# Kernel tuning notes

Hardware: AMD Instinct MI355X
Metric: run time of the kernel (lower is better)

The kernel has to match this reference:

```python
import jax, jax.numpy as jnp
import numpy as np

N = 50000        # nodes
E = 800000       # edges (avg degree 16)
C_IN = 128
H = 256          # hidden_channels
C_OUT = 128
DEPTH = 4
K = 2            # k_hops -> K+1 = 3 TAGConv weight matrices
L = DEPTH - 1    # residual layers after layer-0 conv
EPS = 1e-5
SLOPE = 0.01     # LeakyReLU default negative slope


def setup_inputs() -> dict:
    key = jax.random.key(0)
    ks = iter(jax.random.split(key, 24))
    s = 0.02
    x = jax.random.normal(next(ks), (N, C_IN), dtype=jnp.float32)
    edge_index = jax.random.randint(next(ks), (2, E), 0, N, dtype=jnp.int64)
    edge_weight = jax.random.uniform(next(ks), (E,), dtype=jnp.float32)
    return {
        'x': x,
        'edge_index': edge_index,
        'edge_weight': edge_weight,
        'W_emb': jax.random.normal(next(ks), (C_IN, H)) * s,
        'b_emb': jnp.zeros((H,), jnp.float32),
        'conv0_W': jax.random.normal(next(ks), (K + 1, H, H)) * s,
        'conv0_b': jnp.zeros((H,), jnp.float32),
        'norm_g': jnp.ones((L, H), jnp.float32),
        'norm_b': jnp.zeros((L, H), jnp.float32),
        'conv_W': jax.random.normal(next(ks), (L, K + 1, H, H)) * s,
        'conv_b': jnp.zeros((L, H), jnp.float32),
        'mlp_W1': jax.random.normal(next(ks), (L, H, 4 * H)) * s,
        'mlp_b1': jnp.zeros((L, 4 * H), jnp.float32),
        'mlp_g': jnp.ones((L, 4 * H), jnp.float32),
        'mlp_bb': jnp.zeros((L, 4 * H), jnp.float32),
        'mlp_W2': jax.random.normal(next(ks), (L, 4 * H, H)) * s,
        'mlp_b2': jnp.zeros((L, H), jnp.float32),
        'W_out': jax.random.normal(next(ks), (H, C_OUT)) * s,
        'b_out': jnp.zeros((C_OUT,), jnp.float32),
    }


def _bn(h, g, b):
    # BatchNorm1d over node dim (training-mode batch statistics)
    m = h.mean(axis=0)
    v = h.var(axis=0)
    return g * (h - m) * jax.lax.rsqrt(v + EPS) + b


def _tagconv(h, src, dst, ew, Ws, b):
    # TAGConv (normalize=False, no self loops): sum_k (A^k h) W_k + b
    out = h @ Ws[0]
    p = h
    for k in range(1, Ws.shape[0]):
        msg = p[src] * ew[:, None]                      # [E, H] gather
        p = jax.ops.segment_sum(msg, dst, num_segments=h.shape[0])
        out = out + p @ Ws[k]
    return out + b


def reference(x, edge_index, edge_weight, W_emb, b_emb, conv0_W, conv0_b,
              norm_g, norm_b, conv_W, conv_b, mlp_W1, mlp_b1, mlp_g, mlp_bb,
              mlp_W2, mlp_b2, W_out, b_out):
    src, dst = edge_index[0], edge_index[1]
    h = x @ W_emb + b_emb                               # x_embed (t=None)
    h = _tagconv(h, src, dst, edge_weight, conv0_W, conv0_b)  # layer-0 conv only
    for l in range(norm_g.shape[0]):                    # res+ blocks
        z = jax.nn.leaky_relu(_bn(h, norm_g[l], norm_b[l]), SLOPE)
        z = _tagconv(z, src, dst, edge_weight, conv_W[l], conv_b[l])
        # pyg MLP [H, 4H, H]: Linear -> BN -> act -> Linear (plain last)
        z = jax.nn.leaky_relu(_bn(z @ mlp_W1[l] + mlp_b1[l], mlp_g[l], mlp_bb[l]), SLOPE)
        z = z @ mlp_W2[l] + mlp_b2[l]
        h = h + z                                       # residual (res=Identity)
    return h @ W_out + b_out
```

## Files before the change

kernel.cpp:

```cpp
#include <hip/hip_runtime.h>

#define HDIM 256
#define EPSV 1e-5f
#define SLOPEV 0.01f

typedef __bf16 bf16;
typedef bf16  bf16x8 __attribute__((ext_vector_type(8)));
typedef bf16  bf16x4 __attribute__((ext_vector_type(4)));
typedef float f32x4  __attribute__((ext_vector_type(4)));

#define GLD16(g, l) __builtin_amdgcn_global_load_lds( \
    (const __attribute__((address_space(1))) void*)(g), \
    (__attribute__((address_space(3))) void*)(l), 16, 0, 0)

template<bool STORE_BF16, bool STATS, bool FUSE_BN>
__global__ __launch_bounds__(256, 5)
void gemm_bt_k(const bf16* A0, const bf16* A1, const bf16* A2, const bf16* A3,
               int nseg, int segK,
               const bf16* __restrict__ Wt,
               const float* __restrict__ bias, const bf16* __restrict__ addb,
               void* out0, void* out1, void* out2, void* out3, int ldo,
               int n_store, float* part, int n_stats,
               const float* __restrict__ fcoef)
{
    __shared__ char smem[24576];

    const int tid = threadIdx.x;
    const int wave = tid >> 6, lane = tid & 63;
    const int quad = lane >> 4, l16 = lane & 15;
    const int waveM = (wave >> 1) * 32, waveN = (wave & 1) * 64;

    int bid = blockIdx.y * gridDim.x + blockIdx.x;
    const int nwg = gridDim.x * gridDim.y;
    if ((nwg & 7) == 0) {
        const int cpx = nwg >> 3;
        bid = (bid & 7) * cpx + (bid >> 3);
    }
    const int bx = bid % gridDim.x, by = bid / gridDim.x;
    const int bm = by * 64, bn = bx * 128;
    const int K = nseg * segK;

    const bf16* segs[4] = {A0, A1, A2, A3};
    const int srow = tid >> 2;
    const int skof = (tid & 3) * 8;

    f32x4 acc[2][4] = {};

    const int T = K >> 5;

    bf16x8 aReg;
    float4 ca0, ca1, cd0, cd1;

    auto loadA = [&](int s, int kt) {
        const bf16* gA = segs[s] + (size_t)(bm + srow) * segK + kt + skof;
        aReg = *(const bf16x8*)gA;
        int g = s * segK + kt + skof;
        ca0 = *(const float4*)(fcoef + g);
        ca1 = *(const float4*)(fcoef + g + 4);
        cd0 = *(const float4*)(fcoef + K + g);
        cd1 = *(const float4*)(fcoef + K + g + 4);
    };
    auto applyA = [&](int b) {
        float av[8] = {ca0.x, ca0.y, ca0.z, ca0.w, ca1.x, ca1.y, ca1.z, ca1.w};
        float dv[8] = {cd0.x, cd0.y, cd0.z, cd0.w, cd1.x, cd1.y, cd1.z, cd1.w};
        bf16x8 z;
#pragma unroll
        for (int u = 0; u < 8; ++u) {
            float f = fmaf((float)aReg[u], av[u], dv[u]);
            f = f > 0.f ? f : SLOPEV * f;
            z[u] = (bf16)f;
        }
        *(bf16x8*)(smem + b * 4096 + tid * 16) = z;
    };
    auto stageA_lds = [&](int s, int kt, int b) {
        const bf16* gA = segs[s] + (size_t)(bm + srow) * segK + kt + skof;
        GLD16(gA, smem + b * 4096 + wave * 1024);
    };
    auto stageB = [&](int s, int kt, int b) {
        const bf16* gB = Wt + (size_t)(bn + srow) * K + s * segK + kt + skof;
        char* lB = smem + 8192 + b * 8192 + wave * 1024;
        GLD16(gB,                  lB);
        GLD16(gB + (size_t)64 * K, lB + 4096);
    };

    if (FUSE_BN) loadA(0, 0); else stageA_lds(0, 0, 0);
    stageB(0, 0, 0);
    if (FUSE_BN) applyA(0);
    __syncthreads();

    int s = 0, kt = 0;
    for (int t = 0; t < T; ++t) {
        int s2 = s, kt2 = kt + 32;
        if (kt2 == segK) { s2++; kt2 = 0; }
        if (t + 1 < T) {
            if (FUSE_BN) loadA(s2, kt2); else stageA_lds(s2, kt2, (t + 1) & 1);
            stageB(s2, kt2, (t + 1) & 1);
        }

        const bf16* pa = (const bf16*)(smem + (t & 1) * 4096)
                         + (waveM + l16) * 32 + quad * 8;
        const bf16* pb = (const bf16*)(smem + 8192 + (t & 1) * 8192)
                         + (waveN + l16) * 32 + quad * 8;
        bf16x8 a0 = *(const bf16x8*)(pa);
        bf16x8 a1 = *(const bf16x8*)(pa + 16 * 32);
        bf16x8 b0 = *(const bf16x8*)(pb);
        bf16x8 b1 = *(const bf16x8*)(pb + 16 * 32);
        bf16x8 b2 = *(const bf16x8*)(pb + 32 * 32);
        bf16x8 b3 = *(const bf16x8*)(pb + 48 * 32);

        acc[0][0] = __builtin_amdgcn_mfma_f32_16x16x32_bf16(a0, b0, acc[0][0], 0, 0, 0);
        acc[0][1] = __builtin_amdgcn_mfma_f32_16x16x32_bf16(a0, b1, acc[0][1], 0, 0, 0);
        acc[0][2] = __builtin_amdgcn_mfma_f32_16x16x32_bf16(a0, b2, acc[0][2], 0, 0, 0);
        acc[0][3] = __builtin_amdgcn_mfma_f32_16x16x32_bf16(a0, b3, acc[0][3], 0, 0, 0);
        acc[1][0] = __builtin_amdgcn_mfma_f32_16x16x32_bf16(a1, b0, acc[1][0], 0, 0, 0);
        acc[1][1] = __builtin_amdgcn_mfma_f32_16x16x32_bf16(a1, b1, acc[1][1], 0, 0, 0);
        acc[1][2] = __builtin_amdgcn_mfma_f32_16x16x32_bf16(a1, b2, acc[1][2], 0, 0, 0);
        acc[1][3] = __builtin_amdgcn_mfma_f32_16x16x32_bf16(a1, b3, acc[1][3], 0, 0, 0);

        if (FUSE_BN && t + 1 < T) applyA((t + 1) & 1);
        __syncthreads();
        s = s2; kt = kt2;
    }

    float bv[4];
#pragma unroll
    for (int j = 0; j < 4; ++j)
        bv[j] = bias ? bias[bn + waveN + j * 16 + l16] : 0.f;
#pragma unroll
    for (int i = 0; i < 2; ++i)
#pragma unroll
        for (int j = 0; j < 4; ++j)
#pragma unroll
            for (int r = 0; r < 4; ++r)
                acc[i][j][r] += bv[j];

    void* outs[4] = {out0, out1, out2, out3};

    if (STORE_BF16) {
        char* stg = smem + wave * 4608;
        float s8[8] = {}, q8[8] = {};
        const int rsel = lane >> 3, csel = lane & 7;
#pragma unroll
        for (int i = 0; i < 2; ++i)
#pragma unroll
            for (int j = 0; j < 4; ++j)
#pragma unroll
                for (int r = 0; r < 4; ++r)
                    *(bf16*)(stg + ((i * 16 + quad * 4 + r) * 72 + j * 16 + l16) * 2)
                        = (bf16)acc[i][j][r];
#pragma unroll
        for (int rr = 0; rr < 4; ++rr) {
            int rl = rsel + rr * 8;
            bf16x8 v = *(const bf16x8*)(stg + (rl * 72 + csel * 8) * 2);
            int rowg = bm + waveM + rl;
            int colg = bn + waveN + csel * 8;
            int cseg = colg >> 8, cloc = colg & 255;
            size_t idx = (size_t)rowg * ldo + cloc;
            float f[8];
#pragma unroll
            for (int u = 0; u < 8; ++u) f[u] = (float)v[u];
            if (addb) {
                bf16x8 o = *(const bf16x8*)(addb + idx);
#pragma unroll
                for (int u = 0; u < 8; ++u) f[u] += (float)o[u];
            }
            bf16x8 w;
#pragma unroll
            for (int u = 0; u < 8; ++u) w[u] = (bf16)f[u];
            if (rowg < n_store) *(bf16x8*)((bf16*)outs[cseg] + idx) = w;
            if (STATS && rowg < n_stats) {
#pragma unroll
                for (int u = 0; u < 8; ++u) { s8[u] += f[u]; q8[u] += f[u] * f[u]; }
            }
        }
        if (STATS) {
#pragma unroll
            for (int m = 8; m <= 32; m <<= 1)
#pragma unroll
                for (int u = 0; u < 8; ++u) {
                    s8[u] += __shfl_xor(s8[u], m, 64);
                    q8[u] += __shfl_xor(q8[u], m, 64);
                }
            float* Ls = (float*)(smem + 18432);
            float* Lq = Ls + 256;
            if (rsel == 0) {
#pragma unroll
                for (int u = 0; u < 8; ++u) {
                    Ls[wave * 64 + csel * 8 + u] = s8[u];
                    Lq[wave * 64 + csel * 8 + u] = q8[u];
                }
            }
            __syncthreads();
            if (tid < 128) {
                int hi = tid >> 6, c6 = tid & 63;
                float sv = Ls[hi * 64 + c6] + Ls[(hi + 2) * 64 + c6];
                float qv = Lq[hi * 64 + c6] + Lq[(hi + 2) * 64 + c6];
                int Mtot = gridDim.x * 128;
                int colg = bn + tid;
                part[(size_t)by * Mtot + colg] = sv;
                part[(size_t)(gridDim.y + by) * Mtot + colg] = qv;
            }
        }
    } else {
#pragma unroll
        for (int i = 0; i < 2; ++i)
#pragma unroll
            for (int j = 0; j < 4; ++j) {
                int colg = bn + waveN + j * 16 + l16;
                int cseg = colg >> 8, cloc = colg & 255;
#pragma unroll
                for (int r = 0; r < 4; ++r) {
                    int rowg = bm + waveM + i * 16 + quad * 4 + r;
                    if (rowg < n_store)
                        ((float*)outs[cseg])[(size_t)rowg * ldo + cloc] = acc[i][j][r];
                }
            }
    }
}

__global__ __launch_bounds__(256)
void finalize_k(const float* __restrict__ part, int GY, int M,
                const float* __restrict__ g, const float* __restrict__ bb,
                float* __restrict__ coef, float invn)
{
    const int c = blockIdx.x;
    const int t = threadIdx.x;
    float s = 0.f, q = 0.f;
    const float* ps = part + c;
    const float* pq = part + (size_t)GY * M + c;
    for (int i = t; i < GY; i += 256) {
        s += ps[(size_t)i * M];
        q += pq[(size_t)i * M];
    }
#pragma unroll
    for (int m = 1; m <= 32; m <<= 1) {
        s += __shfl_xor(s, m, 64);
        q += __shfl_xor(q, m, 64);
    }
    __shared__ float Ls[4], Lq[4];
    const int w = t >> 6, l = t & 63;
    if (l == 0) { Ls[w] = s; Lq[w] = q; }
    __syncthreads();
    if (t == 0) {
        s = Ls[0] + Ls[1] + Ls[2] + Ls[3];
        q = Lq[0] + Lq[1] + Lq[2] + Lq[3];
        float mean = s * invn;
        float var  = q * invn - mean * mean;
        float a = g[c] * rsqrtf(var + EPSV);
        coef[c]     = a;
        coef[M + c] = bb[c] - mean * a;
    }
}

__global__ __launch_bounds__(256)
void transpose_cvt_k(const float* __restrict__ src, bf16* __restrict__ dst,
                     int Kseg, int M, int G)
{
    __shared__ float t[32][33];
    const int z = blockIdx.z;
    src += (size_t)z * Kseg * M;
    const int ldd = G * Kseg;
    dst += (size_t)(z / G) * M * ldd + (size_t)(z % G) * Kseg;
    const int tM = blockIdx.x * 32, tK = blockIdx.y * 32;
    const int tx = threadIdx.x & 31, ty = threadIdx.x >> 5;
#pragma unroll
    for (int r = 0; r < 4; ++r)
        t[ty + r * 8][tx] = src[(size_t)(tK + ty + r * 8) * M + tM + tx];
    __syncthreads();
#pragma unroll
    for (int r = 0; r < 4; ++r)
        dst[(size_t)(tM + ty + r * 8) * ldd + tK + tx] = (bf16)t[tx][ty + r * 8];
}

__global__ __launch_bounds__(256)
void cvt_bf_k(const float* __restrict__ src, bf16* __restrict__ dst, long n4)
{
    long i = (long)blockIdx.x * blockDim.x + threadIdx.x;
    if (i >= n4) return;
    float4 v = ((const float4*)src)[i];
    bf16x4 o; o[0] = (bf16)v.x; o[1] = (bf16)v.y; o[2] = (bf16)v.z; o[3] = (bf16)v.w;
    ((bf16x4*)dst)[i] = o;
}

__global__ __launch_bounds__(256)
void deg_k(const int* __restrict__ dst, int* __restrict__ deg, int E)
{
    int e = blockIdx.x * blockDim.x + threadIdx.x;
    if (e < E) atomicAdd(&deg[dst[e]], 1);
}

__global__ __launch_bounds__(256)
void blocksum_k(const int* __restrict__ deg, int* __restrict__ bsum, int N)
{
    int i = blockIdx.x * 256 + threadIdx.x;
    int v = (i < N) ? deg[i] : 0;
#pragma unroll
    for (int m = 1; m <= 32; m <<= 1) v += __shfl_xor(v, m, 64);
    __shared__ int Ls[4];
    if ((threadIdx.x & 63) == 0) Ls[threadIdx.x >> 6] = v;
    __syncthreads();
    if (threadIdx.x == 0) bsum[blockIdx.x] = Ls[0] + Ls[1] + Ls[2] + Ls[3];
}

__global__ __launch_bounds__(256)
void topscan_k(const int* __restrict__ bsum, int* __restrict__ boff, int nb)
{
    __shared__ int s[256];
    int t = threadIdx.x;
    int v = (t < nb) ? bsum[t] : 0;
    s[t] = v;
    __syncthreads();
    for (int off = 1; off < 256; off <<= 1) {
        int u = (t >= off) ? s[t - off] : 0;
        __syncthreads();
        s[t] += u;
        __syncthreads();
    }
    if (t < nb) boff[t] = s[t] - v;
}

__global__ __launch_bounds__(256)
void scatterscan_k(int* __restrict__ deg_wp, const int* __restrict__ boff,
                   int* __restrict__ rowptr, int N)
{
    __shared__ int s[256];
    int t = threadIdx.x;
    int i = blockIdx.x * 256 + t;
    int v = (i < N) ? deg_wp[i] : 0;
    s[t] = v;
    __syncthreads();
    for (int off = 1; off < 256; off <<= 1) {
        int u = (t >= off) ? s[t - off] : 0;
        __syncthreads();
        s[t] += u;
        __syncthreads();
    }
    if (i < N) {
        int incl = s[t] + boff[blockIdx.x];
        rowptr[i + 1] = incl;
        deg_wp[i] = incl - v;
        if (i == 0) rowptr[0] = 0;
    }
}

__global__ __launch_bounds__(256)
void reorder_k(const int* __restrict__ src, const int* __restrict__ dst,
               const float* __restrict__ ew, int* __restrict__ wp,
               int* __restrict__ col, float* __restrict__ wgt, int E)
{
    int e = blockIdx.x * blockDim.x + threadIdx.x;
    if (e >= E) return;
    int d = dst[e];
    int pos = atomicAdd(&wp[d], 1);
    col[pos] = src[e];
    wgt[pos] = ew[e];
}

__global__ __launch_bounds__(256)
void spmm_pull_k(const bf16* __restrict__ P, const int* __restrict__ rowptr,
                 const int* __restrict__ col, const float* __restrict__ wgt,
                 bf16* __restrict__ Q, int N)
{
    int node = blockIdx.x * 8 + (threadIdx.x >> 5);
    int l = threadIdx.x & 31;
    if (node >= N) return;
    int e = rowptr[node], end = rowptr[node + 1];
    float acc[8] = {};
    for (; e + 3 < end; e += 4) {
        int   s0 = col[e],     s1 = col[e + 1], s2 = col[e + 2], s3 = col[e + 3];
        float w0 = wgt[e],     w1 = wgt[e + 1], w2 = wgt[e + 2], w3 = wgt[e + 3];
        bf16x8 v0 = *(const bf16x8*)(P + (size_t)s0 * HDIM + l * 8);
        bf16x8 v1 = *(const bf16x8*)(P + (size_t)s1 * HDIM + l * 8);
        bf16x8 v2 = *(const bf16x8*)(P + (size_t)s2 * HDIM + l * 8);
        bf16x8 v3 = *(const bf16x8*)(P + (size_t)s3 * HDIM + l * 8);
#pragma unroll
        for (int u = 0; u < 8; ++u)
            acc[u] += ((float)v0[u] * w0 + (float)v1[u] * w1)
                    + ((float)v2[u] * w2 + (float)v3[u] * w3);
    }
    for (; e + 1 < end; e += 2) {
        int   s0 = col[e], s1 = col[e + 1];
        float w0 = wgt[e], w1 = wgt[e + 1];
        bf16x8 v0 = *(const bf16x8*)(P + (size_t)s0 * HDIM + l * 8);
        bf16x8 v1 = *(const bf16x8*)(P + (size_t)s1 * HDIM + l * 8);
#pragma unroll
        for (int u = 0; u < 8; ++u)
            acc[u] += (float)v0[u] * w0 + (float)v1[u] * w1;
    }
    if (e < end) {
        int s0 = col[e]; float w0 = wgt[e];
        bf16x8 v0 = *(const bf16x8*)(P + (size_t)s0 * HDIM + l * 8);
#pragma unroll
        for (int u = 0; u < 8; ++u) acc[u] += (float)v0[u] * w0;
    }
    bf16x8 o;
#pragma unroll
    for (int u = 0; u < 8; ++u) o[u] = (bf16)acc[u];
    *(bf16x8*)(Q + (size_t)node * HDIM + l * 8) = o;
}

__global__ __launch_bounds__(256)
void apply_bn_k(const bf16* __restrict__ X, const float* __restrict__ coef,
                bf16* __restrict__ Y, int n)
{
    __shared__ float aL[256], bL[256];
    const int tid = threadIdx.x;
    aL[tid] = coef[tid]; bL[tid] = coef[256 + tid];
    __syncthreads();
    long n4 = (long)n * 64;
    for (long i = (long)blockIdx.x * 256 + tid; i < n4; i += (long)gridDim.x * 256) {
        bf16x4 v = ((const bf16x4*)X)[i];
        int c4 = (int)(i & 63) * 4;
        float r0 = fmaf((float)v[0], aL[c4 + 0], bL[c4 + 0]); r0 = r0 > 0.f ? r0 : SLOPEV * r0;
        float r1 = fmaf((float)v[1], aL[c4 + 1], bL[c4 + 1]); r1 = r1 > 0.f ? r1 : SLOPEV * r1;
        float r2 = fmaf((float)v[2], aL[c4 + 2], bL[c4 + 2]); r2 = r2 > 0.f ? r2 : SLOPEV * r2;
        float r3 = fmaf((float)v[3], aL[c4 + 3], bL[c4 + 3]); r3 = r3 > 0.f ? r3 : SLOPEV * r3;
        bf16x4 o; o[0] = (bf16)r0; o[1] = (bf16)r1; o[2] = (bf16)r2; o[3] = (bf16)r3;
        ((bf16x4*)Y)[i] = o;
    }
}

struct GemmArgs {
    const bf16 *A0, *A1, *A2, *A3; int nseg, segK;
    const bf16* Wt; const float* bias; const bf16* addb;
    void *o0, *o1, *o2, *o3; int ldo, M, n_store;
    float* part; int n_stats;
    const float* fuse;
};

static void gemm(hipStream_t st, const GemmArgs& a, int GYr, bool store_bf16, bool stats)
{
    dim3 g(a.M / 128, GYr), b(256);
    if (a.fuse) {
        if (stats)
            gemm_bt_k<true, true, true><<<g, b, 0, st>>>(a.A0, a.A1, a.A2, a.A3,
                a.nseg, a.segK, a.Wt, a.bias, a.addb, a.o0, a.o1, a.o2, a.o3,
                a.ldo, a.n_store, a.part, a.n_stats, a.fuse);
        else
            gemm_bt_k<true, false, true><<<g, b, 0, st>>>(a.A0, a.A1, a.A2, a.A3,
                a.nseg, a.segK, a.Wt, a.bias, a.addb, a.o0, a.o1, a.o2, a.o3,
                a.ldo, a.n_store, a.part, a.n_stats, a.fuse);
    } else if (store_bf16) {
        if (stats)
            gemm_bt_k<true, true, false><<<g, b, 0, st>>>(a.A0, a.A1, a.A2, a.A3,
                a.nseg, a.segK, a.Wt, a.bias, a.addb, a.o0, a.o1, a.o2, a.o3,
                a.ldo, a.n_store, a.part, a.n_stats, nullptr);
        else
            gemm_bt_k<true, false, false><<<g, b, 0, st>>>(a.A0, a.A1, a.A2, a.A3,
                a.nseg, a.segK, a.Wt, a.bias, a.addb, a.o0, a.o1, a.o2, a.o3,
                a.ldo, a.n_store, a.part, a.n_stats, nullptr);
    } else {
        gemm_bt_k<false, false, false><<<g, b, 0, st>>>(a.A0, a.A1, a.A2, a.A3,
            a.nseg, a.segK, a.Wt, a.bias, a.addb, a.o0, a.o1, a.o2, a.o3,
            a.ldo, a.n_store, a.part, a.n_stats, nullptr);
    }
}

extern "C" void kernel_launch(void* const* d_in, const int* in_sizes, int n_in,
                              void* d_out, int out_size, void* d_ws, size_t ws_size,
                              hipStream_t stream)
{
    const float* x       = (const float*)d_in[0];
    const int*   ei      = (const int*)d_in[1];
    const float* ew      = (const float*)d_in[2];
    const float* W_emb   = (const float*)d_in[3];
    const float* b_emb   = (const float*)d_in[4];
    const float* conv0_W = (const float*)d_in[5];
    const float* conv0_b = (const float*)d_in[6];
    const float* norm_g  = (const float*)d_in[7];
    const float* norm_b  = (const float*)d_in[8];
    const float* conv_W  = (const float*)d_in[9];
    const float* conv_b  = (const float*)d_in[10];
    const float* mlp_W1  = (const float*)d_in[11];
    const float* mlp_b1  = (const float*)d_in[12];
    const float* mlp_g   = (const float*)d_in[13];
    const float* mlp_bb  = (const float*)d_in[14];
    const float* mlp_W2  = (const float*)d_in[15];
    const float* mlp_b2  = (const float*)d_in[16];
    const float* W_out   = (const float*)d_in[17];
    const float* b_out   = (const float*)d_in[18];

    const int N = in_sizes[0] / 128;
    const int E = in_sizes[2];
    const int* srcI = ei;
    const int* dstI = ei + E;
    const int N_pad = ((N + 127) / 128) * 128;
    const int GYr = N_pad / 64;
    const int NB = (N + 255) / 256;

    const size_t NHp = (size_t)N_pad * HDIM;
    bf16* xb = (bf16*)d_ws;
    bf16* hb = xb + (size_t)N_pad * 128;
    bf16* cb = hb + NHp;
    bf16* p1 = cb + NHp;
    bf16* p2 = p1 + NHp;
    bf16* e1 = p2 + NHp;
    bf16* e2 = e1 + NHp;
    bf16* wa = e2 + NHp;
    bf16* Wt_emb   = wa;
    bf16* Wt_conv0 = wa + 32768;
    bf16* Wt_conv  = wa + 229376;
    bf16* Wt_mlp1  = wa + 819200;
    bf16* Wt_mlp2  = wa + 1605632;
    bf16* Wt_out   = wa + 2392064;
    float* cf_h   = (float*)(wa + 2424832);
    float* cf_m   = cf_h + 512;
    float* partb  = cf_m + 2048;
    int*   rowptr = (int*)(partb + 2 * (size_t)GYr * 1024);
    int*   wp     = rowptr + (N + 1);
    int*   col    = wp + N;
    float* wgt    = (float*)(col + E);
    int*   bsum   = (int*)(wgt + E);
    int*   boff   = bsum + 256;

    const float invn = 1.0f / (float)N;
    dim3 pg((N + 7) / 8), pb(256);

    hipMemsetAsync(wp, 0, (size_t)N * 4, stream);
    deg_k<<<dim3((E + 255) / 256), dim3(256), 0, stream>>>(dstI, wp, E);
    blocksum_k<<<dim3(NB), dim3(256), 0, stream>>>(wp, bsum, N);
    topscan_k<<<dim3(1), dim3(256), 0, stream>>>(bsum, boff, NB);
    scatterscan_k<<<dim3(NB), dim3(256), 0, stream>>>(wp, boff, rowptr, N);
    reorder_k<<<dim3((E + 255) / 256), dim3(256), 0, stream>>>(srcI, dstI, ew, wp, col, wgt, E);

    cvt_bf_k<<<dim3((N * 32 + 255) / 256), dim3(256), 0, stream>>>(x, xb, (long)N * 32);
    transpose_cvt_k<<<dim3(8, 4, 1), dim3(256), 0, stream>>>(W_emb, Wt_emb, 128, 256, 1);
    transpose_cvt_k<<<dim3(8, 8, 3), dim3(256), 0, stream>>>(conv0_W, Wt_conv0, 256, 256, 3);
    transpose_cvt_k<<<dim3(8, 8, 9), dim3(256), 0, stream>>>(conv_W, Wt_conv, 256, 256, 3);
    transpose_cvt_k<<<dim3(32, 8, 3), dim3(256), 0, stream>>>(mlp_W1, Wt_mlp1, 256, 1024, 1);
    transpose_cvt_k<<<dim3(8, 32, 3), dim3(256), 0, stream>>>(mlp_W2, Wt_mlp2, 1024, 256, 1);
    transpose_cvt_k<<<dim3(4, 8, 1), dim3(256), 0, stream>>>(W_out, Wt_out, 256, 128, 1);

    {
        GemmArgs a{xb, xb, xb, xb, 1, 128, Wt_emb, b_emb, nullptr,
                   cb, cb, cb, cb, HDIM, 256, N_pad, nullptr, 0, nullptr};
        gemm(stream, a, GYr, true, false);
    }

    spmm_pull_k<<<pg, pb, 0, stream>>>(cb, rowptr, col, wgt, p1, N);
    spmm_pull_k<<<pg, pb, 0, stream>>>(p1, rowptr, col, wgt, p2, N);
    {
        GemmArgs a{cb, p1, p2, p2, 3, 256, Wt_conv0, conv0_b, nullptr,
                   hb, hb, hb, hb, HDIM, 256, N_pad, partb, N, nullptr};
        gemm(stream, a, GYr, true, true);
    }
    finalize_k<<<dim3(256), dim3(256), 0, stream>>>(partb, GYr, 256, norm_g, norm_b, cf_h, invn);

    for (int l = 0; l < 3; ++l) {
        apply_bn_k<<<dim3(1024), dim3(256), 0, stream>>>(hb, cf_h, e1, N);

        spmm_pull_k<<<pg, pb, 0, stream>>>(e1, rowptr, col, wgt, p1, N);
        spmm_pull_k<<<pg, pb, 0, stream>>>(p1, rowptr, col, wgt, p2, N);
        {
            GemmArgs a{e1, p1, p2, p2, 3, 256, Wt_conv + (size_t)l * 196608,
                       conv_b + l * 256, nullptr, cb, cb, cb, cb, HDIM, 256, N_pad,
                       nullptr, 0, nullptr};
            gemm(stream, a, GYr, true, false);
        }

        {
            GemmArgs a{cb, cb, cb, cb, 1, 256, Wt_mlp1 + (size_t)l * 262144,
                       mlp_b1 + (size_t)l * 1024, nullptr, p1, p2, e1, e2, HDIM, 1024,
                       N_pad, partb, N, nullptr};
            gemm(stream, a, GYr, true, true);
        }
        finalize_k<<<dim3(1024), dim3(256), 0, stream>>>(partb, GYr, 1024,
                                                         mlp_g + (size_t)l * 1024,
                                                         mlp_bb + (size_t)l * 1024, cf_m, invn);

        {
            GemmArgs a{p1, p2, e1, e2, 4, 256, Wt_mlp2 + (size_t)l * 262144,
                       mlp_b2 + l * 256, hb, hb, hb, hb, hb, HDIM, 256, N_pad,
                       (l < 2) ? partb : nullptr, N, cf_m};
            gemm(stream, a, GYr, true, l < 2);
        }
        if (l < 2)
            finalize_k<<<dim3(256), dim3(256), 0, stream>>>(partb, GYr, 256,
                                                            norm_g + (l + 1) * 256,
                                                            norm_b + (l + 1) * 256, cf_h, invn);
    }

    {
        GemmArgs a{hb, hb, hb, hb, 1, 256, Wt_out, b_out, nullptr,
                   d_out, d_out, d_out, d_out, 128, 128, N, nullptr, 0, nullptr};
        gemm(stream, a, GYr, false, false);
    }
}
```

Before: 1.377 ms.

## Fuse BN+LeakyReLU into SpMM gather and GEMM A-operand path, drop apply_bn kernel

Removes the standalone apply_bn kernel by applying the BatchNorm affine and LeakyReLU on the fly: in the first SpMM of each layer, to every gathered neighbor row, and in the conv GEMM, to the first A segment after it is read from LDS. The MLP2 GEMM also switches from register-staged A with a pre-applied transform to async global-to-LDS staging, with coefficients cached in shared memory and the transform applied after the LDS read. This avoids writing and re-reading a normalized copy of h each layer. In exchange the SpMM does per-edge extra FMAs, the GEMM now repeats the transform in every column block, and shared memory per block grows.

```diff
diff --git a/kernel.cpp b/kernel.cpp
--- a/kernel.cpp
+++ b/kernel.cpp
@@ -13,7 +13,7 @@
     (const __attribute__((address_space(1))) void*)(g), \
     (__attribute__((address_space(3))) void*)(l), 16, 0, 0)
 
-template<bool STORE_BF16, bool STATS, bool FUSE_BN>
+template<bool STORE_BF16, bool STATS, bool FUSE_A>
 __global__ __launch_bounds__(256, 5)
 void gemm_bt_k(const bf16* A0, const bf16* A1, const bf16* A2, const bf16* A3,
                int nseg, int segK,
@@ -21,9 +21,10 @@
                const float* __restrict__ bias, const bf16* __restrict__ addb,
                void* out0, void* out1, void* out2, void* out3, int ldo,
                int n_store, float* part, int n_stats,
-               const float* __restrict__ fcoef)
-{
-    __shared__ char smem[24576];
+               const float* __restrict__ fcoef, int fuse_nseg, int ncoef)
+{
+    constexpr int SMEMSZ = FUSE_A ? 32768 : 24576;
+    __shared__ char smem[SMEMSZ];
 
     const int tid = threadIdx.x;
     const int wave = tid >> 6, lane = tid & 63;
@@ -48,31 +49,7 @@
 
     const int T = K >> 5;
 
-    bf16x8 aReg;
-    float4 ca0, ca1, cd0, cd1;
-
-    auto loadA = [&](int s, int kt) {
-        const bf16* gA = segs[s] + (size_t)(bm + srow) * segK + kt + skof;
-        aReg = *(const bf16x8*)gA;
-        int g = s * segK + kt + skof;
-        ca0 = *(const float4*)(fcoef + g);
-        ca1 = *(const float4*)(fcoef + g + 4);
-        cd0 = *(const float4*)(fcoef + K + g);
-        cd1 = *(const float4*)(fcoef + K + g + 4);
-    };
-    auto applyA = [&](int b) {
-        float av[8] = {ca0.x, ca0.y, ca0.z, ca0.w, ca1.x, ca1.y, ca1.z, ca1.w};
-        float dv[8] = {cd0.x, cd0.y, cd0.z, cd0.w, cd1.x, cd1.y, cd1.z, cd1.w};
-        bf16x8 z;
-#pragma unroll
-        for (int u = 0; u < 8; ++u) {
-            float f = fmaf((float)aReg[u], av[u], dv[u]);
-            f = f > 0.f ? f : SLOPEV * f;
-            z[u] = (bf16)f;
-        }
-        *(bf16x8*)(smem + b * 4096 + tid * 16) = z;
-    };
-    auto stageA_lds = [&](int s, int kt, int b) {
+    auto stageA = [&](int s, int kt, int b) {
         const bf16* gA = segs[s] + (size_t)(bm + srow) * segK + kt + skof;
         GLD16(gA, smem + b * 4096 + wave * 1024);
     };
@@ -83,9 +60,16 @@
         GLD16(gB + (size_t)64 * K, lB + 4096);
     };
 
-    if (FUSE_BN) loadA(0, 0); else stageA_lds(0, 0, 0);
+    if (FUSE_A) {
+        float* aT = (float*)(smem + 24576);
+        float* bT = aT + 1024;
+        for (int i = tid; i < ncoef; i += 256) {
+            aT[i] = fcoef[i];
+            bT[i] = fcoef[ncoef + i];
+        }
+    }
+    stageA(0, 0, 0);
     stageB(0, 0, 0);
-    if (FUSE_BN) applyA(0);
     __syncthreads();
 
     int s = 0, kt = 0;
@@ -93,7 +77,7 @@
         int s2 = s, kt2 = kt + 32;
         if (kt2 == segK) { s2++; kt2 = 0; }
         if (t + 1 < T) {
-            if (FUSE_BN) loadA(s2, kt2); else stageA_lds(s2, kt2, (t + 1) & 1);
+            stageA(s2, kt2, (t + 1) & 1);
             stageB(s2, kt2, (t + 1) & 1);
         }
 
@@ -108,6 +92,26 @@
         bf16x8 b2 = *(const bf16x8*)(pb + 32 * 32);
         bf16x8 b3 = *(const bf16x8*)(pb + 48 * 32);
 
+        if (FUSE_A && s < fuse_nseg) {
+            const float* aT = (const float*)(smem + 24576);
+            const float* bT = aT + 1024;
+            int kb = s * segK + kt + quad * 8;
+            float av[8], dv[8];
+            *(float4*)(av)     = *(const float4*)(aT + kb);
+            *(float4*)(av + 4) = *(const float4*)(aT + kb + 4);
+            *(float4*)(dv)     = *(const float4*)(bT + kb);
+            *(float4*)(dv + 4) = *(const float4*)(bT + kb + 4);
+#pragma unroll
+            for (int u = 0; u < 8; ++u) {
+                float f0 = fmaf((float)a0[u], av[u], dv[u]);
+                f0 = f0 > 0.f ? f0 : SLOPEV * f0;
+                a0[u] = (bf16)f0;
+                float f1 = fmaf((float)a1[u], av[u], dv[u]);
+                f1 = f1 > 0.f ? f1 : SLOPEV * f1;
+                a1[u] = (bf16)f1;
+            }
+        }
+
         acc[0][0] = __builtin_amdgcn_mfma_f32_16x16x32_bf16(a0, b0, acc[0][0], 0, 0, 0);
         acc[0][1] = __builtin_amdgcn_mfma_f32_16x16x32_bf16(a0, b1, acc[0][1], 0, 0, 0);
         acc[0][2] = __builtin_amdgcn_mfma_f32_16x16x32_bf16(a0, b2, acc[0][2], 0, 0, 0);
@@ -117,7 +121,6 @@
         acc[1][2] = __builtin_amdgcn_mfma_f32_16x16x32_bf16(a1, b2, acc[1][2], 0, 0, 0);
         acc[1][3] = __builtin_amdgcn_mfma_f32_16x16x32_bf16(a1, b3, acc[1][3], 0, 0, 0);
 
-        if (FUSE_BN && t + 1 < T) applyA((t + 1) & 1);
         __syncthreads();
         s = s2; kt = kt2;
     }
@@ -356,14 +359,30 @@
     wgt[pos] = ew[e];
 }
 
+template<bool FUSE>
 __global__ __launch_bounds__(256)
 void spmm_pull_k(const bf16* __restrict__ P, const int* __restrict__ rowptr,
                  const int* __restrict__ col, const float* __restrict__ wgt,
-                 bf16* __restrict__ Q, int N)
+                 bf16* __restrict__ Q, int N, const float* __restrict__ coef)
 {
     int node = blockIdx.x * 8 + (threadIdx.x >> 5);
     int l = threadIdx.x & 31;
     if (node >= N) return;
+    float a8[8], b8[8];
+    if (FUSE) {
+#pragma unroll
+        for (int u = 0; u < 8; ++u) {
+            a8[u] = coef[l * 8 + u];
+            b8[u] = coef[256 + l * 8 + u];
+        }
+    }
+    auto tx = [&](float x, int u) {
+        if (FUSE) {
+            x = fmaf(x, a8[u], b8[u]);
+            x = x > 0.f ? x : SLOPEV * x;
+        }
+        return x;
+    };
     int e = rowptr[node], end = rowptr[node + 1];
     float acc[8] = {};
     for (; e + 3 < end; e += 4) {
@@ -375,8 +394,8 @@
         bf16x8 v3 = *(const bf16x8*)(P + (size_t)s3 * HDIM + l * 8);
 #pragma unroll
         for (int u = 0; u < 8; ++u)
-            acc[u] += ((float)v0[u] * w0 + (float)v1[u] * w1)
-                    + ((float)v2[u] * w2 + (float)v3[u] * w3);
+            acc[u] += (tx((float)v0[u], u) * w0 + tx((float)v1[u], u) * w1)
+                    + (tx((float)v2[u], u) * w2 + tx((float)v3[u], u) * w3);
     }
     for (; e + 1 < end; e += 2) {
         int   s0 = col[e], s1 = col[e + 1];
@@ -385,39 +404,18 @@
         bf16x8 v1 = *(const bf16x8*)(P + (size_t)s1 * HDIM + l * 8);
 #pragma unroll
         for (int u = 0; u < 8; ++u)
-            acc[u] += (float)v0[u] * w0 + (float)v1[u] * w1;
+            acc[u] += tx((float)v0[u], u) * w0 + tx((float)v1[u], u) * w1;
     }
     if (e < end) {
         int s0 = col[e]; float w0 = wgt[e];
         bf16x8 v0 = *(const bf16x8*)(P + (size_t)s0 * HDIM + l * 8);
 #pragma unroll
-        for (int u = 0; u < 8; ++u) acc[u] += (float)v0[u] * w0;
+        for (int u = 0; u < 8; ++u) acc[u] += tx((float)v0[u], u) * w0;
     }
     bf16x8 o;
 #pragma unroll
     for (int u = 0; u < 8; ++u) o[u] = (bf16)acc[u];
     *(bf16x8*)(Q + (size_t)node * HDIM + l * 8) = o;
-}
-
-__global__ __launch_bounds__(256)
-void apply_bn_k(const bf16* __restrict__ X, const float* __restrict__ coef,
-                bf16* __restrict__ Y, int n)
-{
-    __shared__ float aL[256], bL[256];
-    const int tid = threadIdx.x;
-    aL[tid] = coef[tid]; bL[tid] = coef[256 + tid];
-    __syncthreads();
-    long n4 = (long)n * 64;
-    for (long i = (long)blockIdx.x * 256 + tid; i < n4; i += (long)gridDim.x * 256) {
-        bf16x4 v = ((const bf16x4*)X)[i];
-        int c4 = (int)(i & 63) * 4;
-        float r0 = fmaf((float)v[0], aL[c4 + 0], bL[c4 + 0]); r0 = r0 > 0.f ? r0 : SLOPEV * r0;
-        float r1 = fmaf((float)v[1], aL[c4 + 1], bL[c4 + 1]); r1 = r1 > 0.f ? r1 : SLOPEV * r1;
-        float r2 = fmaf((float)v[2], aL[c4 + 2], bL[c4 + 2]); r2 = r2 > 0.f ? r2 : SLOPEV * r2;
-        float r3 = fmaf((float)v[3], aL[c4 + 3], bL[c4 + 3]); r3 = r3 > 0.f ? r3 : SLOPEV * r3;
-        bf16x4 o; o[0] = (bf16)r0; o[1] = (bf16)r1; o[2] = (bf16)r2; o[3] = (bf16)r3;
-        ((bf16x4*)Y)[i] = o;
-    }
 }
 
 struct GemmArgs {
@@ -425,7 +423,7 @@
     const bf16* Wt; const float* bias; const bf16* addb;
     void *o0, *o1, *o2, *o3; int ldo, M, n_store;
     float* part; int n_stats;
-    const float* fuse;
+    const float* fuse; int fuse_nseg; int ncoef;
 };
 
 static void gemm(hipStream_t st, const GemmArgs& a, int GYr, bool store_bf16, bool stats)
@@ -435,24 +433,24 @@
         if (stats)
             gemm_bt_k<true, true, true><<<g, b, 0, st>>>(a.A0, a.A1, a.A2, a.A3,
                 a.nseg, a.segK, a.Wt, a.bias, a.addb, a.o0, a.o1, a.o2, a.o3,
-                a.ldo, a.n_store, a.part, a.n_stats, a.fuse);
+                a.ldo, a.n_store, a.part, a.n_stats, a.fuse, a.fuse_nseg, a.ncoef);
         else
             gemm_bt_k<true, false, true><<<g, b, 0, st>>>(a.A0, a.A1, a.A2, a.A3,
                 a.nseg, a.segK, a.Wt, a.bias, a.addb, a.o0, a.o1, a.o2, a.o3,
-                a.ldo, a.n_store, a.part, a.n_stats, a.fuse);
+                a.ldo, a.n_store, a.part, a.n_stats, a.fuse, a.fuse_nseg, a.ncoef);
     } else if (store_bf16) {
         if (stats)
             gemm_bt_k<true, true, false><<<g, b, 0, st>>>(a.A0, a.A1, a.A2, a.A3,
                 a.nseg, a.segK, a.Wt, a.bias, a.addb, a.o0, a.o1, a.o2, a.o3,
-                a.ldo, a.n_store, a.part, a.n_stats, nullptr);
+                a.ldo, a.n_store, a.part, a.n_stats, nullptr, 0, 0);
         else
             gemm_bt_k<true, false, false><<<g, b, 0, st>>>(a.A0, a.A1, a.A2, a.A3,
                 a.nseg, a.segK, a.Wt, a.bias, a.addb, a.o0, a.o1, a.o2, a.o3,
-                a.ldo, a.n_store, a.part, a.n_stats, nullptr);
+                a.ldo, a.n_store, a.part, a.n_stats, nullptr, 0, 0);
     } else {
         gemm_bt_k<false, false, false><<<g, b, 0, st>>>(a.A0, a.A1, a.A2, a.A3,
             a.nseg, a.segK, a.Wt, a.bias, a.addb, a.o0, a.o1, a.o2, a.o3,
-            a.ldo, a.n_store, a.part, a.n_stats, nullptr);
+            a.ldo, a.n_store, a.part, a.n_stats, nullptr, 0, 0);
     }
 }
 
@@ -533,35 +531,33 @@
 
     {
         GemmArgs a{xb, xb, xb, xb, 1, 128, Wt_emb, b_emb, nullptr,
-                   cb, cb, cb, cb, HDIM, 256, N_pad, nullptr, 0, nullptr};
+                   cb, cb, cb, cb, HDIM, 256, N_pad, nullptr, 0, nullptr, 0, 0};
         gemm(stream, a, GYr, true, false);
     }
 
-    spmm_pull_k<<<pg, pb, 0, stream>>>(cb, rowptr, col, wgt, p1, N);
-    spmm_pull_k<<<pg, pb, 0, stream>>>(p1, rowptr, col, wgt, p2, N);
+    spmm_pull_k<false><<<pg, pb, 0, stream>>>(cb, rowptr, col, wgt, p1, N, nullptr);
+    spmm_pull_k<false><<<pg, pb, 0, stream>>>(p1, rowptr, col, wgt, p2, N, nullptr);
     {
         GemmArgs a{cb, p1, p2, p2, 3, 256, Wt_conv0, conv0_b, nullptr,
-                   hb, hb, hb, hb, HDIM, 256, N_pad, partb, N, nullptr};
+                   hb, hb, hb, hb, HDIM, 256, N_pad, partb, N, nullptr, 0, 0};
         gemm(stream, a, GYr, true, true);
     }
     finalize_k<<<dim3(256), dim3(256), 0, stream>>>(partb, GYr, 256, norm_g, norm_b, cf_h, invn);
 
     for (int l = 0; l < 3; ++l) {
-        apply_bn_k<<<dim3(1024), dim3(256), 0, stream>>>(hb, cf_h, e1, N);
-
-        spmm_pull_k<<<pg, pb, 0, stream>>>(e1, rowptr, col, wgt, p1, N);
-        spmm_pull_k<<<pg, pb, 0, stream>>>(p1, rowptr, col, wgt, p2, N);
+        spmm_pull_k<true><<<pg, pb, 0, stream>>>(hb, rowptr, col, wgt, p1, N, cf_h);
+        spmm_pull_k<false><<<pg, pb, 0, stream>>>(p1, rowptr, col, wgt, p2, N, nullptr);
         {
-            GemmArgs a{e1, p1, p2, p2, 3, 256, Wt_conv + (size_t)l * 196608,
+            GemmArgs a{hb, p1, p2, p2, 3, 256, Wt_conv + (size_t)l * 196608,
                        conv_b + l * 256, nullptr, cb, cb, cb, cb, HDIM, 256, N_pad,
-                       nullptr, 0, nullptr};
+                       nullptr, 0, cf_h, 1, 256};
             gemm(stream, a, GYr, true, false);
         }
 
         {
             GemmArgs a{cb, cb, cb, cb, 1, 256, Wt_mlp1 + (size_t)l * 262144,
                        mlp_b1 + (size_t)l * 1024, nullptr, p1, p2, e1, e2, HDIM, 1024,
-                       N_pad, partb, N, nullptr};
+                       N_pad, partb, N, nullptr, 0, 0};
             gemm(stream, a, GYr, true, true);
         }
         finalize_k<<<dim3(1024), dim3(256), 0, stream>>>(partb, GYr, 1024,
@@ -571,7 +567,7 @@
         {
             GemmArgs a{p1, p2, e1, e2, 4, 256, Wt_mlp2 + (size_t)l * 262144,
                        mlp_b2 + l * 256, hb, hb, hb, hb, hb, HDIM, 256, N_pad,
-                       (l < 2) ? partb : nullptr, N, cf_m};
+                       (l < 2) ? partb : nullptr, N, cf_m, 4, 1024};
             gemm(stream, a, GYr, true, l < 2);
         }
         if (l < 2)
@@ -582,7 +578,7 @@
 
     {
         GemmArgs a{hb, hb, hb, hb, 1, 256, Wt_out, b_out, nullptr,
-                   d_out, d_out, d_out, d_out, 128, 128, N, nullptr, 0, nullptr};
+                   d_out, d_out, d_out, d_out, 128, 128, N, nullptr, 0, nullptr, 0, 0};
         gemm(stream, a, GYr, false, false);
     }
 }
```

New measurement: 1.381 ms. Within noise of the previous version (+0.3%).
